# Performance work log

Hardware: AMD Instinct MI355X
Metric: run time of the kernel (lower is better)

The kernel has to match this reference:

```python
import jax, jax.numpy as jnp
import numpy as np

K = 8192          # num_codes
D = 256           # code_dim
COMMIT_BETA = 0.25


def setup_inputs() -> dict:
    key = jax.random.key(0)
    k1, k2 = jax.random.split(key)
    z_e = jax.random.normal(k1, (16, 2048, D), dtype=jnp.float32)
    # nn.init.normal_(weight, mean=0, std=1/sqrt(D))
    codebook = jax.random.normal(k2, (K, D), dtype=jnp.float32) * (1.0 / D ** 0.5)
    return {"z_e": z_e, "codebook": codebook}


def reference(z_e, codebook):
    lead_shape = z_e.shape[:-1]
    flat = z_e.reshape(-1, D)                                   # (N, D)
    dist = (
        jnp.sum(flat * flat, axis=-1, keepdims=True)
        - 2.0 * flat @ codebook.T
        + jnp.sum(codebook * codebook, axis=-1)
    )
    idx = jnp.argmin(dist, axis=-1).reshape(lead_shape)          # (...,) int
    z_q = codebook[idx]                                          # (..., D)
    codebook_loss = jnp.mean((z_q - jax.lax.stop_gradient(z_e)) ** 2)
    commit_loss = jnp.mean((z_e - jax.lax.stop_gradient(z_q)) ** 2)
    loss = codebook_loss + COMMIT_BETA * commit_loss
    # straight-through estimator
    z_q_ste = z_e + jax.lax.stop_gradient(z_q - z_e)
    return z_q_ste, idx, loss
```

## Files before the change

### kernel.cpp

```cpp
#include <hip/hip_runtime.h>


#define N_TOK   32768
#define KC      8192
#define DD      256
#define D4      64
#define CSPL    4
#define MT      128
#define EPS1    0.025f
#define EPS2    1e-3f
#define FLAG_CAP 8192
#define CAP2     4096
#define ASTR    40

typedef __bf16    bf16x8 __attribute__((ext_vector_type(8)));
typedef _Float16  f16x8  __attribute__((ext_vector_type(8)));
typedef _Float16  f16x4  __attribute__((ext_vector_type(4)));
typedef float     f32x4  __attribute__((ext_vector_type(4)));

#define GLL(gp, lp) __builtin_amdgcn_global_load_lds(                                   \
    (const __attribute__((address_space(1))) void*)(unsigned long long)(uintptr_t)(gp), \
    (__attribute__((address_space(3))) void*)(unsigned)(uintptr_t)(lp), 16, 0, 0)

#define PK(a, b, HO, LO) do {                                   \
    unsigned ua = __float_as_uint(a), ub = __float_as_uint(b);  \
    unsigned ham = ua & 0xFFFF0000u, hbm = ub & 0xFFFF0000u;    \
    float la = (a) - __uint_as_float(ham);                      \
    float lb = (b) - __uint_as_float(hbm);                      \
    HO = (ua >> 16) | hbm;                                      \
    LO = (__float_as_uint(la) >> 16) | (__float_as_uint(lb) & 0xFFFF0000u); \
} while (0)

__global__ __launch_bounds__(256)
void k_cnorm(const float* __restrict__ cb, float* __restrict__ cnorm,
             double* __restrict__ accum, int* __restrict__ flagc,
             int* __restrict__ flagc2, _Float16* __restrict__ cbf16,
             ushort* __restrict__ cbh, ushort* __restrict__ cbl) {
    if (blockIdx.x == 0 && threadIdx.x == 0) { *accum = 0.0; *flagc = 0; *flagc2 = 0; }
    const int gid  = blockIdx.x * 256 + threadIdx.x;
    const int code = gid >> 6;
    const int lane = threadIdx.x & 63;
    if (code < KC) {
        float4 v = ((const float4*)cb)[code * D4 + lane];
        if (cbf16) {
            f16x4 h;
            h[0] = (_Float16)v.x; h[1] = (_Float16)v.y;
            h[2] = (_Float16)v.z; h[3] = (_Float16)v.w;
            *(f16x4*)(cbf16 + (size_t)code * DD + lane * 4) = h;
        }
        if (cbh) {
            unsigned h01, l01, h23, l23;
            PK(v.x, v.y, h01, l01);
            PK(v.z, v.w, h23, l23);
            uint2 hp; hp.x = h01; hp.y = h23;
            uint2 lp; lp.x = l01; lp.y = l23;
            *(uint2*)(cbh + (size_t)code * DD + lane * 4) = hp;
            *(uint2*)(cbl + (size_t)code * DD + lane * 4) = lp;
        }
        float s = v.x*v.x + v.y*v.y + v.z*v.z + v.w*v.w;
        #pragma unroll
        for (int off = 32; off > 0; off >>= 1) s += __shfl_down(s, off);
        if (lane == 0) cnorm[code] = s;
    }
}

__global__ __launch_bounds__(256)
void k_convert_ze(const float* __restrict__ src, _Float16* __restrict__ dst, int n8) {
    int t = blockIdx.x * 256 + threadIdx.x;
    if (t >= n8) return;
    const float4* s = (const float4*)src;
    float4 v0 = s[2 * t], v1 = s[2 * t + 1];
    f16x8 h;
    h[0] = (_Float16)v0.x; h[1] = (_Float16)v0.y; h[2] = (_Float16)v0.z; h[3] = (_Float16)v0.w;
    h[4] = (_Float16)v1.x; h[5] = (_Float16)v1.y; h[6] = (_Float16)v1.z; h[7] = (_Float16)v1.w;
    ((f16x8*)dst)[t] = h;
}

__global__ __launch_bounds__(256, 4)
void k_argmin_f16(const _Float16* __restrict__ zef, const _Float16* __restrict__ cbf,
                  const float* __restrict__ cnorm, float4* __restrict__ partial) {
    __shared__ __align__(16) char smem[32768];

    const int tid  = threadIdx.x;
    const int lane = tid & 63;
    const int wid  = tid >> 6;
    const int cl   = lane & 15;
    const int kq   = lane >> 4;
    const int m0   = blockIdx.x * MT;
    const int split = blockIdx.y;
    const int c0b  = split * (KC / CSPL);
    const int wrow0 = wid * 32;
    const int lr   = lane >> 5;
    const int lc   = lane & 31;

    f16x8 afr[2][8];
    #pragma unroll
    for (int h = 0; h < 2; ++h) {
        #pragma unroll
        for (int j = 0; j < 8; ++j) {
            int I = wid * 8 + j;
            int r = 2 * I + lr;
            int c = lc ^ (r & 31);
            GLL((const char*)zef + (size_t)(m0 + h * 64 + r) * 512 + c * 16,
                smem + I * 1024);
        }
        __syncthreads();
        if ((wid >> 1) == h) {
            #pragma unroll
            for (int mt = 0; mt < 2; ++mt)
                #pragma unroll
                for (int ks = 0; ks < 8; ++ks) {
                    int rr = (wid & 1) * 32 + mt * 16 + cl;
                    int c  = ks * 4 + kq;
                    afr[mt][ks] = *(const f16x8*)(smem + rr * 512 + ((c ^ (rr & 31)) << 4));
                }
        }
        __syncthreads();
    }

    char* bbuf0 = smem;
    char* bbuf1 = smem + 16384;
    unsigned boffs[4];
    #pragma unroll
    for (int j = 0; j < 4; ++j) {
        int I = wid * 4 + j;
        int r = 2 * I + lr;
        boffs[j] = (unsigned)r * 512u + (unsigned)((lc ^ (r & 31)) << 4);
    }

    #pragma unroll
    for (int j = 0; j < 4; ++j)
        GLL((const char*)cbf + (size_t)c0b * 512 + boffs[j], bbuf0 + (wid * 4 + j) * 1024);
    __syncthreads();

    float best[8], sec[8]; int bidx[8];
    #pragma unroll
    for (int s = 0; s < 8; ++s) { best[s] = 3.4e38f; sec[s] = 3.4e38f; bidx[s] = 0; }

    for (int ch = 0; ch < 64; ++ch) {
        char* cur = (ch & 1) ? bbuf1 : bbuf0;
        char* nxt = (ch & 1) ? bbuf0 : bbuf1;
        if (ch < 63) {
            const size_t gb = (size_t)(c0b + (ch + 1) * 32) * 512;
            #pragma unroll
            for (int j = 0; j < 4; ++j)
                GLL((const char*)cbf + gb + boffs[j], nxt + (wid * 4 + j) * 1024);
        }

        f32x4 acc[2][2];
        #pragma unroll
        for (int mt = 0; mt < 2; ++mt)
            #pragma unroll
            for (int nt = 0; nt < 2; ++nt)
                acc[mt][nt] = (f32x4){0.f, 0.f, 0.f, 0.f};

        #pragma unroll
        for (int ks = 0; ks < 8; ++ks) {
            f16x8 bfr[2];
            #pragma unroll
            for (int nt = 0; nt < 2; ++nt) {
                int row = nt * 16 + cl;
                int c   = ks * 4 + kq;
                bfr[nt] = *(const f16x8*)(cur + row * 512 + ((c ^ (row & 31)) << 4));
            }
            #pragma unroll
            for (int mt = 0; mt < 2; ++mt)
                #pragma unroll
                for (int nt = 0; nt < 2; ++nt)
                    acc[mt][nt] = __builtin_amdgcn_mfma_f32_16x16x32_f16(afr[mt][ks], bfr[nt], acc[mt][nt], 0, 0, 0);
        }

        const int cc0 = c0b + ch * 32;
        #pragma unroll
        for (int nt = 0; nt < 2; ++nt) {
            const int code = cc0 + nt * 16 + cl;
            const float cn = cnorm[code];
            #pragma unroll
            for (int mt = 0; mt < 2; ++mt)
                #pragma unroll
                for (int r = 0; r < 4; ++r) {
                    float dist = fmaf(-2.f, acc[mt][nt][r], cn);
                    int s = mt * 4 + r;
                    bool lt = dist < best[s];
                    sec[s] = lt ? best[s] : fminf(sec[s], dist);
                    if (lt) { best[s] = dist; bidx[s] = code; }
                }
        }
        __syncthreads();
    }

    #pragma unroll
    for (int m = 1; m < 16; m <<= 1) {
        #pragma unroll
        for (int s = 0; s < 8; ++s) {
            float ob = __shfl_xor(best[s], m);
            int   oi = __shfl_xor(bidx[s], m);
            float os = __shfl_xor(sec[s], m);
            if (ob < best[s] || (ob == best[s] && oi < bidx[s])) {
                sec[s]  = fminf(best[s], os);
                best[s] = ob; bidx[s] = oi;
            } else {
                sec[s]  = fminf(sec[s], ob);
            }
        }
    }
    if (cl == 0) {
        #pragma unroll
        for (int mt = 0; mt < 2; ++mt)
            #pragma unroll
            for (int r = 0; r < 4; ++r) {
                int row = wrow0 + mt * 16 + kq * 4 + r;
                int s = mt * 4 + r;
                partial[(size_t)split * N_TOK + m0 + row] =
                    make_float4(best[s], __int_as_float(bidx[s]), sec[s], 0.f);
            }
    }
}

__global__ __launch_bounds__(256)
void k_combine(const float4* __restrict__ partial, int* __restrict__ idxi,
               float* __restrict__ idxf, int* __restrict__ flagc,
               int* __restrict__ flag_list, int splits, float eps, int cap) {
    const int t = blockIdx.x * 256 + threadIdx.x;
    float B = 3.4e38f, S = 3.4e38f; int I = 0;
    for (int s = 0; s < splits; ++s) {
        float4 p = partial[(size_t)s * N_TOK + t];
        int oi = __float_as_int(p.y);
        if (p.x < B || (p.x == B && oi < I)) { S = fminf(B, p.z); B = p.x; I = oi; }
        else                                  { S = fminf(S, p.x); }
    }
    idxi[t] = I;
    idxf[t] = (float)I;
    if (S - B < eps) {
        int pos = atomicAdd(flagc, 1);
        if (pos < cap) flag_list[pos] = t;
    }
}

__device__ __forceinline__ void stage8(const float* __restrict__ gp,
                                       ushort* __restrict__ h, ushort* __restrict__ l) {
    float4 v0 = *(const float4*)gp;
    float4 v1 = *(const float4*)(gp + 4);
    uint4 hp, lp;
    PK(v0.x, v0.y, hp.x, lp.x);
    PK(v0.z, v0.w, hp.y, lp.y);
    PK(v1.x, v1.y, hp.z, lp.z);
    PK(v1.z, v1.w, hp.w, lp.w);
    *(uint4*)h = hp;
    *(uint4*)l = lp;
}

__global__ __launch_bounds__(256, 2)
void k_argmin2(const float* __restrict__ ze, const ushort* __restrict__ cbh,
               const ushort* __restrict__ cbl, const float* __restrict__ cnorm,
               const int* __restrict__ flag_list, const int* __restrict__ flagc,
               float4* __restrict__ partial2) {
    int nf = flagc[0]; if (nf > FLAG_CAP) nf = FLAG_CAP;
    const int m0 = blockIdx.x * 64;
    if (m0 >= nf) return;

    __shared__ ushort smem2[(64 + 64 + 256 + 256) * ASTR];
    ushort* Ah = smem2;
    ushort* Al = Ah + 64 * ASTR;
    ushort* Bh = Al + 64 * ASTR;
    ushort* Bl = Bh + 256 * ASTR;

    const int tid  = threadIdx.x;
    const int lane = tid & 63;
    const int wid  = tid >> 6;
    const int cl   = lane & 15;
    const int kq   = lane >> 4;
    const int wn   = wid * 64;
    const int split = blockIdx.y;

    const int r0 = tid >> 2;
    const int g0 = (tid & 3) * 8;
    int tokr = m0 + r0; if (tokr > nf - 1) tokr = nf - 1;
    const int tok = flag_list[tokr];
    const float* zeA = ze + (size_t)tok * DD + g0;

    const int boff = (wn + cl) * ASTR + kq * 8;

    float best[16], sec[16]; int bidx[16];
    #pragma unroll
    for (int s = 0; s < 16; ++s) { best[s] = 3.4e38f; sec[s] = 3.4e38f; bidx[s] = 0; }

    for (int ch = 0; ch < 2; ++ch) {
        const int c0 = split * 512 + ch * 256;
        f32x4 acc[4][4];
        #pragma unroll
        for (int mt = 0; mt < 4; ++mt)
            #pragma unroll
            for (int nt = 0; nt < 4; ++nt)
                acc[mt][nt] = (f32x4){0.f, 0.f, 0.f, 0.f};

        for (int ks = 0; ks < 8; ++ks) {
            __syncthreads();
            stage8(zeA + ks * 32, Ah + r0 * ASTR + g0, Al + r0 * ASTR + g0);
            #pragma unroll
            for (int rep = 0; rep < 4; ++rep) {
                const size_t crow = (size_t)(c0 + rep * 64 + r0) * DD + ks * 32 + g0;
                *(uint4*)(Bh + (r0 + rep * 64) * ASTR + g0) = *(const uint4*)(cbh + crow);
                *(uint4*)(Bl + (r0 + rep * 64) * ASTR + g0) = *(const uint4*)(cbl + crow);
            }
            __syncthreads();

            bf16x8 bh[4], bl[4];
            #pragma unroll
            for (int nt = 0; nt < 4; ++nt) {
                bh[nt] = *(const bf16x8*)(Bh + boff + nt * 16 * ASTR);
                bl[nt] = *(const bf16x8*)(Bl + boff + nt * 16 * ASTR);
            }
            #pragma unroll
            for (int mt = 0; mt < 4; ++mt) {
                const int ao = (mt * 16 + cl) * ASTR + kq * 8;
                bf16x8 ah = *(const bf16x8*)(Ah + ao);
                bf16x8 al = *(const bf16x8*)(Al + ao);
                #pragma unroll
                for (int nt = 0; nt < 4; ++nt) {
                    acc[mt][nt] = __builtin_amdgcn_mfma_f32_16x16x32_bf16(ah, bh[nt], acc[mt][nt], 0, 0, 0);
                    acc[mt][nt] = __builtin_amdgcn_mfma_f32_16x16x32_bf16(ah, bl[nt], acc[mt][nt], 0, 0, 0);
                    acc[mt][nt] = __builtin_amdgcn_mfma_f32_16x16x32_bf16(al, bh[nt], acc[mt][nt], 0, 0, 0);
                }
            }
        }
        #pragma unroll
        for (int nt = 0; nt < 4; ++nt) {
            const int code = c0 + wn + nt * 16 + cl;
            const float cn = cnorm[code];
            #pragma unroll
            for (int mt = 0; mt < 4; ++mt)
                #pragma unroll
                for (int r = 0; r < 4; ++r) {
                    float dist = fmaf(-2.f, acc[mt][nt][r], cn);
                    int s = mt * 4 + r;
                    bool lt = dist < best[s];
                    sec[s] = lt ? best[s] : fminf(sec[s], dist);
                    if (lt) { best[s] = dist; bidx[s] = code; }
                }
        }
    }

    #pragma unroll
    for (int m = 1; m < 16; m <<= 1) {
        #pragma unroll
        for (int s = 0; s < 16; ++s) {
            float ob = __shfl_xor(best[s], m);
            int   oi = __shfl_xor(bidx[s], m);
            float os = __shfl_xor(sec[s], m);
            if (ob < best[s] || (ob == best[s] && oi < bidx[s])) {
                sec[s]  = fminf(best[s], os);
                best[s] = ob; bidx[s] = oi;
            } else {
                sec[s]  = fminf(sec[s], ob);
            }
        }
    }
    __syncthreads();
    float* mg = (float*)smem2;
    if (cl == 0) {
        #pragma unroll
        for (int mt = 0; mt < 4; ++mt)
            #pragma unroll
            for (int r = 0; r < 4; ++r) {
                int row = mt * 16 + kq * 4 + r;
                int o = (wid * 64 + row) * 4;
                mg[o + 0] = best[mt * 4 + r];
                mg[o + 1] = __int_as_float(bidx[mt * 4 + r]);
                mg[o + 2] = sec[mt * 4 + r];
            }
    }
    __syncthreads();
    if (tid < 64 && m0 + tid < nf) {
        float B = 3.4e38f, S = 3.4e38f; int I = 0;
        #pragma unroll
        for (int j = 0; j < 4; ++j) {
            float b = mg[(j * 64 + tid) * 4];
            int   i = __float_as_int(mg[(j * 64 + tid) * 4 + 1]);
            float s = mg[(j * 64 + tid) * 4 + 2];
            if (b < B || (b == B && i < I)) { S = fminf(B, s); B = b; I = i; }
            else                             { S = fminf(S, b); }
        }
        partial2[(size_t)split * FLAG_CAP + m0 + tid] = make_float4(B, __int_as_float(I), S, 0.f);
    }
}

__global__ __launch_bounds__(256)
void k_combine2(const float4* __restrict__ partial2, const int* __restrict__ flag_list,
                const int* __restrict__ flagc, int* __restrict__ idxi,
                float* __restrict__ idxf, int* __restrict__ flagc2,
                int* __restrict__ list2) {
    int nf = flagc[0]; if (nf > FLAG_CAP) nf = FLAG_CAP;
    const int f = blockIdx.x * 256 + threadIdx.x;
    if (f >= nf) return;
    float B = 3.4e38f, S = 3.4e38f; int I = 0;
    #pragma unroll
    for (int s = 0; s < 16; ++s) {
        float4 p = partial2[(size_t)s * FLAG_CAP + f];
        int oi = __float_as_int(p.y);
        if (p.x < B || (p.x == B && oi < I)) { S = fminf(B, p.z); B = p.x; I = oi; }
        else                                  { S = fminf(S, p.x); }
    }
    const int t = flag_list[f];
    idxi[t] = I;
    idxf[t] = (float)I;
    if (S - B < EPS2) {
        int pos = atomicAdd(flagc2, 1);
        if (pos < CAP2) list2[pos] = t;
    }
}

__global__ __launch_bounds__(256)
void k_rescore_part(const float* __restrict__ ze, const float* __restrict__ cb,
                    const float* __restrict__ cnorm, const int* __restrict__ flagc,
                    const int* __restrict__ flag_list, float2* __restrict__ part3,
                    int cap) {
    __shared__ float xsh[DD];
    __shared__ float2 red[256];
    const int tid = threadIdx.x;
    const int cs  = blockIdx.y;
    int nf = flagc[0]; if (nf > cap) nf = cap;
    for (int f = blockIdx.x; f < nf; f += gridDim.x) {
        const int t = flag_list[f];
        if (tid < 64) *(float4*)&xsh[tid * 4] = ((const float4*)ze)[(size_t)t * D4 + tid];
        __syncthreads();
        const int c = cs * 256 + tid;
        const float4* cr = (const float4*)(cb + (size_t)c * DD);
        float dot = 0.f;
        #pragma unroll 8
        for (int j = 0; j < D4; ++j) {
            float4 cv = cr[j];
            float4 xv = *(const float4*)&xsh[j * 4];
            dot = fmaf(cv.x, xv.x, dot);
            dot = fmaf(cv.y, xv.y, dot);
            dot = fmaf(cv.z, xv.z, dot);
            dot = fmaf(cv.w, xv.w, dot);
        }
        red[tid] = make_float2(fmaf(-2.f, dot, cnorm[c]), __int_as_float(c));
        __syncthreads();
        for (int s = 128; s > 0; s >>= 1) {
            if (tid < s) {
                float2 o = red[tid + s], me = red[tid];
                int oi = __float_as_int(o.y), mi = __float_as_int(me.y);
                if (o.x < me.x || (o.x == me.x && oi < mi)) red[tid] = o;
            }
            __syncthreads();
        }
        if (tid == 0) part3[(size_t)f * 32 + cs] = red[0];
        __syncthreads();
    }
}

__global__ __launch_bounds__(256)
void k_rescore_fin(const float2* __restrict__ part3, const int* __restrict__ flagc,
                   const int* __restrict__ flag_list, int* __restrict__ idxi,
                   float* __restrict__ idxf, int cap) {
    int nf = flagc[0]; if (nf > cap) nf = cap;
    const int f = blockIdx.x * 256 + threadIdx.x;
    if (f >= nf) return;
    float B = 3.4e38f; int I = 0;
    #pragma unroll
    for (int s = 0; s < 32; ++s) {
        float2 p = part3[(size_t)f * 32 + s];
        int oi = __float_as_int(p.y);
        if (p.x < B || (p.x == B && oi < I)) { B = p.x; I = oi; }
    }
    const int t = flag_list[f];
    idxi[t] = I;
    idxf[t] = (float)I;
}

__global__ __launch_bounds__(256)
void k_rescore(const float* __restrict__ ze, const float* __restrict__ cb,
               const float* __restrict__ cnorm, const int* __restrict__ flagc,
               const int* __restrict__ flag_list, int* __restrict__ idxi,
               float* __restrict__ idxf, int cap) {
    __shared__ float xsh[DD];
    __shared__ float2 red[256];
    const int tid = threadIdx.x;
    int nf = flagc[0]; if (nf > cap) nf = cap;
    for (int f = blockIdx.x; f < nf; f += gridDim.x) {
        const int t = flag_list[f];
        if (tid < 64) *(float4*)&xsh[tid * 4] = ((const float4*)ze)[(size_t)t * D4 + tid];
        __syncthreads();
        float B = 3.4e38f; int I = 0;
        for (int c = tid; c < KC; c += 256) {
            const float4* cr = (const float4*)(cb + (size_t)c * DD);
            float dot = 0.f;
            #pragma unroll 8
            for (int j = 0; j < D4; ++j) {
                float4 cv = cr[j];
                float4 xv = *(const float4*)&xsh[j * 4];
                dot = fmaf(cv.x, xv.x, dot);
                dot = fmaf(cv.y, xv.y, dot);
                dot = fmaf(cv.z, xv.z, dot);
                dot = fmaf(cv.w, xv.w, dot);
            }
            float dist = fmaf(-2.f, dot, cnorm[c]);
            if (dist < B) { B = dist; I = c; }
        }
        red[tid] = make_float2(B, __int_as_float(I));
        __syncthreads();
        for (int s = 128; s > 0; s >>= 1) {
            if (tid < s) {
                float2 o = red[tid + s], me = red[tid];
                int oi = __float_as_int(o.y), mi = __float_as_int(me.y);
                if (o.x < me.x || (o.x == me.x && oi < mi)) red[tid] = o;
            }
            __syncthreads();
        }
        if (tid == 0) { int I2 = __float_as_int(red[0].y); idxi[t] = I2; idxf[t] = (float)I2; }
        __syncthreads();
    }
}

__global__ __launch_bounds__(256)
void k_gather(const float* __restrict__ ze, const float* __restrict__ cb,
              const int* __restrict__ idxi, float* __restrict__ zq,
              double* __restrict__ accum) {
    const int tid = threadIdx.x;
    const int t0  = blockIdx.x * 16;
    double dsum = 0.0;
    #pragma unroll
    for (int i = 0; i < 4; ++i) {
        int f = tid + i * 256;
        int row = f >> 6, e = f & 63;
        int t = t0 + row;
        int code = idxi[t];
        float4 zev = ((const float4*)ze)[(size_t)t * D4 + e];
        float4 cbv = ((const float4*)cb)[(size_t)code * D4 + e];
        float dx = cbv.x - zev.x, dy = cbv.y - zev.y;
        float dz = cbv.z - zev.z, dw = cbv.w - zev.w;
        float4 o;
        o.x = zev.x + dx; o.y = zev.y + dy; o.z = zev.z + dz; o.w = zev.w + dw;
        ((float4*)zq)[(size_t)t * D4 + e] = o;
        dsum += (double)dx * dx + (double)dy * dy + (double)dz * dz + (double)dw * dw;
    }
    #pragma unroll
    for (int off = 32; off > 0; off >>= 1) dsum += __shfl_down(dsum, off);
    __shared__ double wsum[4];
    if ((tid & 63) == 0) wsum[tid >> 6] = dsum;
    __syncthreads();
    if (tid == 0) atomicAdd(accum, wsum[0] + wsum[1] + wsum[2] + wsum[3]);
}

__global__ void k_final(const double* __restrict__ accum, float* __restrict__ loss) {
    loss[0] = (float)(accum[0] * (1.25 / 8388608.0));
}

__global__ __launch_bounds__(256, 2)
void k_argmin_fb(const float* __restrict__ ze, const float* __restrict__ cb,
                 const float* __restrict__ cnorm, float4* __restrict__ partial) {
    __shared__ ushort smem[4 * 128 * ASTR];
    ushort* Ah = smem;
    ushort* Al = smem + 128 * ASTR;
    ushort* Bh = smem + 2 * 128 * ASTR;
    ushort* Bl = smem + 3 * 128 * ASTR;

    const int tid  = threadIdx.x;
    const int lane = tid & 63;
    const int wid  = tid >> 6;
    const int cl   = lane & 15;
    const int kq   = lane >> 4;
    const int wm   = (wid & 1) * 64;
    const int wn   = (wid >> 1) * 64;
    const int m0   = blockIdx.x * MT;
    const int split = blockIdx.y;

    const int r0 = tid >> 2;
    const int g0 = (tid & 3) * 8;
    const float* zeA = ze + (size_t)(m0 + r0) * DD + g0;
    const int aoff = (wm + cl) * ASTR + kq * 8;
    const int boff = (wn + cl) * ASTR + kq * 8;

    float best[16], sec[16]; int bidx[16];
    #pragma unroll
    for (int s = 0; s < 16; ++s) { best[s] = 3.4e38f; sec[s] = 3.4e38f; bidx[s] = 0; }

    for (int ch = 0; ch < 4; ++ch) {
        const int c0 = split * 512 + ch * 128;
        const float* cbB = cb + (size_t)(c0 + r0) * DD + g0;
        f32x4 acc[4][4];
        #pragma unroll
        for (int mt = 0; mt < 4; ++mt)
            #pragma unroll
            for (int nt = 0; nt < 4; ++nt)
                acc[mt][nt] = (f32x4){0.f, 0.f, 0.f, 0.f};

        for (int ks = 0; ks < 8; ++ks) {
            __syncthreads();
            stage8(zeA + ks * 32,            Ah + r0 * ASTR + g0, Al + r0 * ASTR + g0);
            stage8(zeA + 64 * DD + ks * 32,  Ah + (r0 + 64) * ASTR + g0, Al + (r0 + 64) * ASTR + g0);
            stage8(cbB + ks * 32,            Bh + r0 * ASTR + g0, Bl + r0 * ASTR + g0);
            stage8(cbB + 64 * DD + ks * 32,  Bh + (r0 + 64) * ASTR + g0, Bl + (r0 + 64) * ASTR + g0);
            __syncthreads();

            bf16x8 bh[4], bl[4];
            #pragma unroll
            for (int nt = 0; nt < 4; ++nt) {
                bh[nt] = *(const bf16x8*)(Bh + boff + nt * 16 * ASTR);
                bl[nt] = *(const bf16x8*)(Bl + boff + nt * 16 * ASTR);
            }
            #pragma unroll
            for (int mt = 0; mt < 4; ++mt) {
                bf16x8 ah = *(const bf16x8*)(Ah + aoff + mt * 16 * ASTR);
                bf16x8 al = *(const bf16x8*)(Al + aoff + mt * 16 * ASTR);
                #pragma unroll
                for (int nt = 0; nt < 4; ++nt) {
                    acc[mt][nt] = __builtin_amdgcn_mfma_f32_16x16x32_bf16(ah, bh[nt], acc[mt][nt], 0, 0, 0);
                    acc[mt][nt] = __builtin_amdgcn_mfma_f32_16x16x32_bf16(ah, bl[nt], acc[mt][nt], 0, 0, 0);
                    acc[mt][nt] = __builtin_amdgcn_mfma_f32_16x16x32_bf16(al, bh[nt], acc[mt][nt], 0, 0, 0);
                }
            }
        }
        #pragma unroll
        for (int nt = 0; nt < 4; ++nt) {
            const int code = c0 + wn + nt * 16 + cl;
            const float cn = cnorm[code];
            #pragma unroll
            for (int mt = 0; mt < 4; ++mt)
                #pragma unroll
                for (int r = 0; r < 4; ++r) {
                    float dist = fmaf(-2.f, acc[mt][nt][r], cn);
                    int s = mt * 4 + r;
                    bool lt = dist < best[s];
                    sec[s] = lt ? best[s] : fminf(sec[s], dist);
                    if (lt) { best[s] = dist; bidx[s] = code; }
                }
        }
    }

    #pragma unroll
    for (int m = 1; m < 16; m <<= 1) {
        #pragma unroll
        for (int s = 0; s < 16; ++s) {
            float ob = __shfl_xor(best[s], m);
            int   oi = __shfl_xor(bidx[s], m);
            float os = __shfl_xor(sec[s], m);
            if (ob < best[s] || (ob == best[s] && oi < bidx[s])) {
                sec[s]  = fminf(best[s], os);
                best[s] = ob; bidx[s] = oi;
            } else {
                sec[s]  = fminf(sec[s], ob);
            }
        }
    }
    __syncthreads();
    float* mg = (float*)smem;
    if (cl == 0) {
        #pragma unroll
        for (int mt = 0; mt < 4; ++mt)
            #pragma unroll
            for (int r = 0; r < 4; ++r) {
                int row = wm + mt * 16 + kq * 4 + r;
                int o = ((wn >> 6) * 128 + row) * 4;
                mg[o + 0] = best[mt * 4 + r];
                mg[o + 1] = __int_as_float(bidx[mt * 4 + r]);
                mg[o + 2] = sec[mt * 4 + r];
            }
    }
    __syncthreads();
    if (tid < MT) {
        float b0 = mg[tid * 4],         s0v = mg[tid * 4 + 2];
        int   i0 = __float_as_int(mg[tid * 4 + 1]);
        float b1 = mg[(128 + tid) * 4], s1v = mg[(128 + tid) * 4 + 2];
        int   i1 = __float_as_int(mg[(128 + tid) * 4 + 1]);
        float B, S; int I;
        if (b1 < b0 || (b1 == b0 && i1 < i0)) { B = b1; I = i1; S = fminf(s1v, b0); }
        else                                   { B = b0; I = i0; S = fminf(s0v, b1); }
        partial[(size_t)split * N_TOK + m0 + tid] = make_float4(B, __int_as_float(I), S, 0.f);
    }
}

extern "C" void kernel_launch(void* const* d_in, const int* in_sizes, int n_in,
                              void* d_out, int out_size, void* d_ws, size_t ws_size,
                              hipStream_t stream) {
    const float* ze = (const float*)d_in[0];
    const float* cb = (const float*)d_in[1];

    float* out      = (float*)d_out;
    float* out_zq   = out;
    float* out_idx  = out + (size_t)N_TOK * DD;
    float* out_loss = out_idx + N_TOK;

    char*   ws    = (char*)d_ws;
    float*  cnorm = (float*)ws;
    int*    idxi  = (int*)(ws + 32768);
    double* accum = (double*)(ws + 163840);
    int*    flagc = (int*)(ws + 163848);
    int*    flagc2= (int*)(ws + 163852);
    int*    flag_list = (int*)(ws + 163856);
    int*    list2     = (int*)(ws + 196624);

    const size_t OFF_ZEF  = 213008;
    const size_t OFF_CBF  = OFF_ZEF + (size_t)N_TOK * DD * 2;
    const size_t OFF_P1   = OFF_CBF + (size_t)KC * DD * 2;
    const size_t OFF_P2   = OFF_P1 + (size_t)CSPL * N_TOK * 16;
    const size_t OFF_P3   = OFF_P2 + 16ull * FLAG_CAP * 16;
    const size_t OFF_CBH  = OFF_P3 + (size_t)CAP2 * 32 * 8;
    const size_t OFF_CBL  = OFF_CBH + (size_t)KC * DD * 2;
    const size_t NEED     = OFF_CBL + (size_t)KC * DD * 2;

    if (ws_size >= NEED) {
        _Float16* zef = (_Float16*)(ws + OFF_ZEF);
        _Float16* cbf = (_Float16*)(ws + OFF_CBF);
        float4* partial  = (float4*)(ws + OFF_P1);
        float4* partial2 = (float4*)(ws + OFF_P2);
        float2* part3    = (float2*)(ws + OFF_P3);
        ushort* cbh = (ushort*)(ws + OFF_CBH);
        ushort* cbl = (ushort*)(ws + OFF_CBL);

        hipLaunchKernelGGL(k_cnorm, dim3(KC / 4), dim3(256), 0, stream,
                           cb, cnorm, accum, flagc, flagc2, cbf, cbh, cbl);
        hipLaunchKernelGGL(k_convert_ze, dim3(N_TOK * DD / 8 / 256), dim3(256), 0, stream,
                           ze, zef, N_TOK * DD / 8);
        hipLaunchKernelGGL(k_argmin_f16, dim3(N_TOK / MT, CSPL), dim3(256), 0, stream,
                           zef, cbf, cnorm, partial);
        hipLaunchKernelGGL(k_combine, dim3(N_TOK / 256), dim3(256), 0, stream,
                           partial, idxi, out_idx, flagc, flag_list, CSPL, EPS1, FLAG_CAP);
        hipLaunchKernelGGL(k_argmin2, dim3(FLAG_CAP / 64, 16), dim3(256), 0, stream,
                           ze, cbh, cbl, cnorm, flag_list, flagc, partial2);
        hipLaunchKernelGGL(k_combine2, dim3(FLAG_CAP / 256), dim3(256), 0, stream,
                           partial2, flag_list, flagc, idxi, out_idx, flagc2, list2);
        hipLaunchKernelGGL(k_rescore_part, dim3(64, 32), dim3(256), 0, stream,
                           ze, cb, cnorm, flagc2, list2, part3, CAP2);
        hipLaunchKernelGGL(k_rescore_fin, dim3(CAP2 / 256), dim3(256), 0, stream,
                           part3, flagc2, list2, idxi, out_idx, CAP2);
    } else {
        hipLaunchKernelGGL(k_cnorm, dim3(KC / 4), dim3(256), 0, stream,
                           cb, cnorm, accum, flagc, flagc2, (_Float16*)0, (ushort*)0, (ushort*)0);
        float4* partial = (float4*)d_out;
        int* fl = (int*)(ws + 163856);
        hipLaunchKernelGGL(k_argmin_fb, dim3(N_TOK / MT, 16), dim3(256), 0, stream,
                           ze, cb, cnorm, partial);
        hipLaunchKernelGGL(k_combine, dim3(N_TOK / 256), dim3(256), 0, stream,
                           partial, idxi, out_idx, flagc, fl, 16, EPS2, FLAG_CAP);
        hipLaunchKernelGGL(k_rescore, dim3(128), dim3(256), 0, stream,
                           ze, cb, cnorm, flagc, fl, idxi, out_idx, FLAG_CAP);
    }

    hipLaunchKernelGGL(k_gather, dim3(N_TOK / 16), dim3(256), 0, stream, ze, cb, idxi, out_zq, accum);
    hipLaunchKernelGGL(k_final,  dim3(1), dim3(1), 0, stream, accum, out_loss);
}
```

Before: 450.8 us.

## Enlarge argmin token tile to 256 with 512 threads and fuse prep kernels

Each argmin block now covers 256 tokens with 8 waves and stages 64-code chunks of the f16 codebook in a 64KB double buffer. The codebook is split in two instead of four, so each block reuses every staged codebook tile across twice as many rows and writes fewer partial results. The codebook norm/convert kernel and the z_e-to-f16 kernel are merged into one launch to save a launch. In exchange the grid shrinks to 256 blocks, large LDS use limits blocks per CU, and the launch bounds of (512,4) may squeeze the register budget and cause spills.

```diff
diff --git a/kernel.cpp b/kernel.cpp
--- a/kernel.cpp
+++ b/kernel.cpp
@@ -5,8 +5,8 @@
 #define KC      8192
 #define DD      256
 #define D4      64
-#define CSPL    4
-#define MT      128
+#define CSPL    2
+#define MT      256
 #define EPS1    0.025f
 #define EPS2    1e-3f
 #define FLAG_CAP 8192
@@ -32,54 +32,54 @@
 } while (0)
 
 __global__ __launch_bounds__(256)
-void k_cnorm(const float* __restrict__ cb, float* __restrict__ cnorm,
-             double* __restrict__ accum, int* __restrict__ flagc,
-             int* __restrict__ flagc2, _Float16* __restrict__ cbf16,
-             ushort* __restrict__ cbh, ushort* __restrict__ cbl) {
-    if (blockIdx.x == 0 && threadIdx.x == 0) { *accum = 0.0; *flagc = 0; *flagc2 = 0; }
-    const int gid  = blockIdx.x * 256 + threadIdx.x;
+void k_prep(const float* __restrict__ cb, float* __restrict__ cnorm,
+            double* __restrict__ accum, int* __restrict__ flagc,
+            int* __restrict__ flagc2, _Float16* __restrict__ cbf16,
+            ushort* __restrict__ cbh, ushort* __restrict__ cbl,
+            const float* __restrict__ ze, _Float16* __restrict__ zef) {
+    const int b = blockIdx.x;
+    if (b == 0 && threadIdx.x == 0) { *accum = 0.0; *flagc = 0; *flagc2 = 0; }
+    if (b >= 2048) {
+        if (!zef) return;
+        int t = (b - 2048) * 256 + threadIdx.x;
+        if (t >= N_TOK * DD / 8) return;
+        const float4* s = (const float4*)ze;
+        float4 v0 = s[2 * t], v1 = s[2 * t + 1];
+        f16x8 h;
+        h[0] = (_Float16)v0.x; h[1] = (_Float16)v0.y; h[2] = (_Float16)v0.z; h[3] = (_Float16)v0.w;
+        h[4] = (_Float16)v1.x; h[5] = (_Float16)v1.y; h[6] = (_Float16)v1.z; h[7] = (_Float16)v1.w;
+        ((f16x8*)zef)[t] = h;
+        return;
+    }
+    const int gid  = b * 256 + threadIdx.x;
     const int code = gid >> 6;
     const int lane = threadIdx.x & 63;
-    if (code < KC) {
-        float4 v = ((const float4*)cb)[code * D4 + lane];
-        if (cbf16) {
-            f16x4 h;
-            h[0] = (_Float16)v.x; h[1] = (_Float16)v.y;
-            h[2] = (_Float16)v.z; h[3] = (_Float16)v.w;
-            *(f16x4*)(cbf16 + (size_t)code * DD + lane * 4) = h;
-        }
-        if (cbh) {
-            unsigned h01, l01, h23, l23;
-            PK(v.x, v.y, h01, l01);
-            PK(v.z, v.w, h23, l23);
-            uint2 hp; hp.x = h01; hp.y = h23;
-            uint2 lp; lp.x = l01; lp.y = l23;
-            *(uint2*)(cbh + (size_t)code * DD + lane * 4) = hp;
-            *(uint2*)(cbl + (size_t)code * DD + lane * 4) = lp;
-        }
-        float s = v.x*v.x + v.y*v.y + v.z*v.z + v.w*v.w;
-        #pragma unroll
-        for (int off = 32; off > 0; off >>= 1) s += __shfl_down(s, off);
-        if (lane == 0) cnorm[code] = s;
-    }
-}
-
-__global__ __launch_bounds__(256)
-void k_convert_ze(const float* __restrict__ src, _Float16* __restrict__ dst, int n8) {
-    int t = blockIdx.x * 256 + threadIdx.x;
-    if (t >= n8) return;
-    const float4* s = (const float4*)src;
-    float4 v0 = s[2 * t], v1 = s[2 * t + 1];
-    f16x8 h;
-    h[0] = (_Float16)v0.x; h[1] = (_Float16)v0.y; h[2] = (_Float16)v0.z; h[3] = (_Float16)v0.w;
-    h[4] = (_Float16)v1.x; h[5] = (_Float16)v1.y; h[6] = (_Float16)v1.z; h[7] = (_Float16)v1.w;
-    ((f16x8*)dst)[t] = h;
-}
-
-__global__ __launch_bounds__(256, 4)
+    float4 v = ((const float4*)cb)[code * D4 + lane];
+    if (cbf16) {
+        f16x4 h;
+        h[0] = (_Float16)v.x; h[1] = (_Float16)v.y;
+        h[2] = (_Float16)v.z; h[3] = (_Float16)v.w;
+        *(f16x4*)(cbf16 + (size_t)code * DD + lane * 4) = h;
+    }
+    if (cbh) {
+        unsigned h01, l01, h23, l23;
+        PK(v.x, v.y, h01, l01);
+        PK(v.z, v.w, h23, l23);
+        uint2 hp; hp.x = h01; hp.y = h23;
+        uint2 lp; lp.x = l01; lp.y = l23;
+        *(uint2*)(cbh + (size_t)code * DD + lane * 4) = hp;
+        *(uint2*)(cbl + (size_t)code * DD + lane * 4) = lp;
+    }
+    float s = v.x*v.x + v.y*v.y + v.z*v.z + v.w*v.w;
+    #pragma unroll
+    for (int off = 32; off > 0; off >>= 1) s += __shfl_down(s, off);
+    if (lane == 0) cnorm[code] = s;
+}
+
+__global__ __launch_bounds__(512, 4)
 void k_argmin_f16(const _Float16* __restrict__ zef, const _Float16* __restrict__ cbf,
                   const float* __restrict__ cnorm, float4* __restrict__ partial) {
-    __shared__ __align__(16) char smem[32768];
+    __shared__ __align__(16) char smem[65536];
 
     const int tid  = threadIdx.x;
     const int lane = tid & 63;
@@ -95,10 +95,10 @@
 
     f16x8 afr[2][8];
     #pragma unroll
-    for (int h = 0; h < 2; ++h) {
-        #pragma unroll
-        for (int j = 0; j < 8; ++j) {
-            int I = wid * 8 + j;
+    for (int h = 0; h < 4; ++h) {
+        #pragma unroll
+        for (int j = 0; j < 4; ++j) {
+            int I = wid * 4 + j;
             int r = 2 * I + lr;
             int c = lc ^ (r & 31);
             GLL((const char*)zef + (size_t)(m0 + h * 64 + r) * 512 + c * 16,
@@ -119,18 +119,15 @@
     }
 
     char* bbuf0 = smem;
-    char* bbuf1 = smem + 16384;
-    unsigned boffs[4];
+    char* bbuf1 = smem + 32768;
+
     #pragma unroll
     for (int j = 0; j < 4; ++j) {
         int I = wid * 4 + j;
         int r = 2 * I + lr;
-        boffs[j] = (unsigned)r * 512u + (unsigned)((lc ^ (r & 31)) << 4);
-    }
-
-    #pragma unroll
-    for (int j = 0; j < 4; ++j)
-        GLL((const char*)cbf + (size_t)c0b * 512 + boffs[j], bbuf0 + (wid * 4 + j) * 1024);
+        GLL((const char*)cbf + (size_t)(c0b + r) * 512 + ((lc ^ (r & 31)) << 4),
+            bbuf0 + I * 1024);
+    }
     __syncthreads();
 
     float best[8], sec[8]; int bidx[8];
@@ -141,50 +138,57 @@
         char* cur = (ch & 1) ? bbuf1 : bbuf0;
         char* nxt = (ch & 1) ? bbuf0 : bbuf1;
         if (ch < 63) {
-            const size_t gb = (size_t)(c0b + (ch + 1) * 32) * 512;
-            #pragma unroll
-            for (int j = 0; j < 4; ++j)
-                GLL((const char*)cbf + gb + boffs[j], nxt + (wid * 4 + j) * 1024);
-        }
-
-        f32x4 acc[2][2];
-        #pragma unroll
-        for (int mt = 0; mt < 2; ++mt)
-            #pragma unroll
-            for (int nt = 0; nt < 2; ++nt)
-                acc[mt][nt] = (f32x4){0.f, 0.f, 0.f, 0.f};
-
-        #pragma unroll
-        for (int ks = 0; ks < 8; ++ks) {
-            f16x8 bfr[2];
+            const int cr0 = c0b + (ch + 1) * 64;
+            #pragma unroll
+            for (int j = 0; j < 4; ++j) {
+                int I = wid * 4 + j;
+                int r = 2 * I + lr;
+                GLL((const char*)cbf + (size_t)(cr0 + r) * 512 + ((lc ^ (r & 31)) << 4),
+                    nxt + I * 1024);
+            }
+        }
+
+        #pragma unroll
+        for (int half = 0; half < 2; ++half) {
+            f32x4 acc[2][2];
+            #pragma unroll
+            for (int mt = 0; mt < 2; ++mt)
+                #pragma unroll
+                for (int nt = 0; nt < 2; ++nt)
+                    acc[mt][nt] = (f32x4){0.f, 0.f, 0.f, 0.f};
+
+            #pragma unroll
+            for (int ks = 0; ks < 8; ++ks) {
+                f16x8 bfr[2];
+                #pragma unroll
+                for (int nt = 0; nt < 2; ++nt) {
+                    int row = half * 32 + nt * 16 + cl;
+                    int c   = ks * 4 + kq;
+                    bfr[nt] = *(const f16x8*)(cur + row * 512 + ((c ^ (row & 31)) << 4));
+                }
+                #pragma unroll
+                for (int mt = 0; mt < 2; ++mt)
+                    #pragma unroll
+                    for (int nt = 0; nt < 2; ++nt)
+                        acc[mt][nt] = __builtin_amdgcn_mfma_f32_16x16x32_f16(afr[mt][ks], bfr[nt], acc[mt][nt], 0, 0, 0);
+            }
+
+            const int cc0 = c0b + ch * 64 + half * 32;
             #pragma unroll
             for (int nt = 0; nt < 2; ++nt) {
-                int row = nt * 16 + cl;
-                int c   = ks * 4 + kq;
-                bfr[nt] = *(const f16x8*)(cur + row * 512 + ((c ^ (row & 31)) << 4));
-            }
-            #pragma unroll
-            for (int mt = 0; mt < 2; ++mt)
-                #pragma unroll
-                for (int nt = 0; nt < 2; ++nt)
-                    acc[mt][nt] = __builtin_amdgcn_mfma_f32_16x16x32_f16(afr[mt][ks], bfr[nt], acc[mt][nt], 0, 0, 0);
-        }
-
-        const int cc0 = c0b + ch * 32;
-        #pragma unroll
-        for (int nt = 0; nt < 2; ++nt) {
-            const int code = cc0 + nt * 16 + cl;
-            const float cn = cnorm[code];
-            #pragma unroll
-            for (int mt = 0; mt < 2; ++mt)
-                #pragma unroll
-                for (int r = 0; r < 4; ++r) {
-                    float dist = fmaf(-2.f, acc[mt][nt][r], cn);
-                    int s = mt * 4 + r;
-                    bool lt = dist < best[s];
-                    sec[s] = lt ? best[s] : fminf(sec[s], dist);
-                    if (lt) { best[s] = dist; bidx[s] = code; }
-                }
+                const int code = cc0 + nt * 16 + cl;
+                const float cn = cnorm[code];
+                #pragma unroll
+                for (int mt = 0; mt < 2; ++mt)
+                    #pragma unroll
+                    for (int r = 0; r < 4; ++r) {
+                        float dist = fmaf(-2.f, acc[mt][nt][r], cn);
+                        int s = mt * 4 + r;
+                        bool lt = dist < best[s];
+                        sec[s] = lt ? best[s] : fminf(sec[s], dist);
+                        if (lt) { best[s] = dist; bidx[s] = code; }
+                    }
+            }
         }
         __syncthreads();
     }
@@ -564,7 +568,7 @@
     const int kq   = lane >> 4;
     const int wm   = (wid & 1) * 64;
     const int wn   = (wid >> 1) * 64;
-    const int m0   = blockIdx.x * MT;
+    const int m0   = blockIdx.x * 128;
     const int split = blockIdx.y;
 
     const int r0 = tid >> 2;
@@ -660,7 +664,7 @@
             }
     }
     __syncthreads();
-    if (tid < MT) {
+    if (tid < 128) {
         float b0 = mg[tid * 4],         s0v = mg[tid * 4 + 2];
         int   i0 = __float_as_int(mg[tid * 4 + 1]);
         float b1 = mg[(128 + tid) * 4], s1v = mg[(128 + tid) * 4 + 2];
@@ -710,11 +714,9 @@
         ushort* cbh = (ushort*)(ws + OFF_CBH);
         ushort* cbl = (ushort*)(ws + OFF_CBL);
 
-        hipLaunchKernelGGL(k_cnorm, dim3(KC / 4), dim3(256), 0, stream,
-                           cb, cnorm, accum, flagc, flagc2, cbf, cbh, cbl);
-        hipLaunchKernelGGL(k_convert_ze, dim3(N_TOK * DD / 8 / 256), dim3(256), 0, stream,
-                           ze, zef, N_TOK * DD / 8);
-        hipLaunchKernelGGL(k_argmin_f16, dim3(N_TOK / MT, CSPL), dim3(256), 0, stream,
+        hipLaunchKernelGGL(k_prep, dim3(2048 + N_TOK * DD / 8 / 256), dim3(256), 0, stream,
+                           cb, cnorm, accum, flagc, flagc2, cbf, cbh, cbl, ze, zef);
+        hipLaunchKernelGGL(k_argmin_f16, dim3(N_TOK / MT, CSPL), dim3(512), 0, stream,
                            zef, cbf, cnorm, partial);
         hipLaunchKernelGGL(k_combine, dim3(N_TOK / 256), dim3(256), 0, stream,
                            partial, idxi, out_idx, flagc, flag_list, CSPL, EPS1, FLAG_CAP);
@@ -727,11 +729,12 @@
         hipLaunchKernelGGL(k_rescore_fin, dim3(CAP2 / 256), dim3(256), 0, stream,
                            part3, flagc2, list2, idxi, out_idx, CAP2);
     } else {
-        hipLaunchKernelGGL(k_cnorm, dim3(KC / 4), dim3(256), 0, stream,
-                           cb, cnorm, accum, flagc, flagc2, (_Float16*)0, (ushort*)0, (ushort*)0);
+        hipLaunchKernelGGL(k_prep, dim3(2048), dim3(256), 0, stream,
+                           cb, cnorm, accum, flagc, flagc2, (_Float16*)0, (ushort*)0, (ushort*)0,
+                           ze, (_Float16*)0);
         float4* partial = (float4*)d_out;
         int* fl = (int*)(ws + 163856);
-        hipLaunchKernelGGL(k_argmin_fb, dim3(N_TOK / MT, 16), dim3(256), 0, stream,
+        hipLaunchKernelGGL(k_argmin_fb, dim3(N_TOK / 128, 16), dim3(256), 0, stream,
                            ze, cb, cnorm, partial);
         hipLaunchKernelGGL(k_combine, dim3(N_TOK / 256), dim3(256), 0, stream,
                            partial, idxi, out_idx, flagc, fl, 16, EPS2, FLAG_CAP);
```

After: 818.4 us. 1.82x slower.
